# Kernel optimization log

Hardware: AMD Instinct MI355X
Metric: run time of the kernel (lower is better)

The kernel has to match this reference:

```python
import jax, jax.numpy as jnp
import numpy as np

# Sizes derived from init_kwargs via calc_mlp_features:
# total_param=2117777, router_ratio=0.002 -> router_param=4235.554, expert_param=264192
# expert_hidden = 256, router_hidden = 352
N = 131072      # number of coordinate points
CIN = 3         # expert_insize == router_insize (xyz coords)
E = 8           # num_experts
K = 2           # top_k
H = 256         # expert_hidden (also SIREN data_channel)
RH = 352        # router_hidden
NHID = 3        # expert_layers - 2 hidden SIREN layers
W0C = 30.0      # sine frequency w0


def setup_inputs() -> dict:
    key = jax.random.key(0)
    ks = jax.random.split(key, 16)
    u = lambda k, shape, a: jax.random.uniform(k, shape, jnp.float32, -a, a)
    x = jax.random.uniform(ks[0], (N, CIN), jnp.float32, -1.0, 1.0)
    context = jax.random.uniform(ks[1], (N, CIN), jnp.float32, -1.0, 1.0)
    # Router: kaiming-normal weights, torch-default uniform biases
    Wr1 = jax.random.normal(ks[2], (CIN, RH), jnp.float32) * np.float32(np.sqrt(2.0 / CIN))
    br1 = u(ks[3], (RH,), 1.0 / np.sqrt(CIN))
    Wr2 = jax.random.normal(ks[4], (RH, E), jnp.float32) * np.float32(np.sqrt(2.0 / RH))
    br2 = u(ks[5], (E,), 1.0 / np.sqrt(RH))
    # SIREN experts (stacked over E): first layer U(-1/in, 1/in), rest U(+-sqrt(6/in)/30)
    sb = np.sqrt(6.0 / H) / 30.0
    W0 = u(ks[6], (E, CIN, H), 1.0 / CIN)
    b0 = u(ks[7], (E, H), 1.0 / np.sqrt(CIN))
    Wh = u(ks[8], (E, NHID, H, H), sb)
    bh = u(ks[9], (E, NHID, H), 1.0 / np.sqrt(H))
    Wo = u(ks[10], (E, H, H), sb)
    bo = u(ks[11], (E, H), 1.0 / np.sqrt(H))
    # Decoder: Linear(H,H)+ReLU+Linear(H,1)
    Wd1 = jax.random.normal(ks[12], (H, H), jnp.float32) * np.float32(np.sqrt(2.0 / H))
    bd1 = u(ks[13], (H,), 1.0 / np.sqrt(H))
    Wd2 = jax.random.normal(ks[14], (H, 1), jnp.float32) * np.float32(np.sqrt(2.0 / H))
    bd2 = u(ks[15], (1,), 1.0 / np.sqrt(H))
    return dict(x=x, context=context, Wr1=Wr1, br1=br1, Wr2=Wr2, br2=br2,
                W0=W0, b0=b0, Wh=Wh, bh=bh, Wo=Wo, bo=bo,
                Wd1=Wd1, bd1=bd1, Wd2=Wd2, bd2=bd2)


def reference(x, context, Wr1, br1, Wr2, br2, W0, b0, Wh, bh, Wo, bo, Wd1, bd1, Wd2, bd2):
    n = x.shape[0]
    # --- NoisyTopkRouter (eval path: no noise) ---
    logits = jnp.maximum(context @ Wr1 + br1, 0.0) @ Wr2 + br2          # [N, E]
    topv, topi = jax.lax.top_k(logits, K)                                # [N, K]
    # softmax over -inf-filled sparse logits == softmax over the top-k values
    w = jax.nn.softmax(topv, axis=-1)                                    # [N, K]
    gating = jnp.zeros_like(logits).at[jnp.arange(n)[:, None], topi].set(w)  # [N, E], zero off top-k
    # --- Per-expert SIREN, weighted combine ---
    # Masked dispatch + scatter-add in the original equals dense weighted sum
    # because gating is exactly zero for non-selected experts.
    def expert_step(acc, p):
        W0e, b0e, Whe, bhe, Woe, boe, ge = p
        h = jnp.sin(W0C * (x @ W0e + b0e))                # [N, H]
        for i in range(NHID):
            h = jnp.sin(W0C * (h @ Whe[i] + bhe[i]))
        out = h @ Woe + boe                               # [N, H], no output activation
        return acc + out * ge[:, None], None
    acc0 = jnp.zeros((n, H), dtype=x.dtype)
    final, _ = jax.lax.scan(expert_step, acc0, (W0, b0, Wh, bh, Wo, bo, gating.T))
    # --- Decoder ---
    return jnp.maximum(final @ Wd1 + bd1, 0.0) @ Wd2 + bd2               # [N, 1]
```

## Files before the change

### kernel.cpp

```cpp
#include <hip/hip_runtime.h>
#include <stdint.h>

#define N_PTS 131072
#define RH    352
#define BM    256
#define BME   64
#define TPB   512
#define SREV  4.774648292756860f

typedef short  bf16x8 __attribute__((ext_vector_type(8)));
typedef float  f32x16 __attribute__((ext_vector_type(16)));

__device__ __forceinline__ unsigned short f2bf(float f) {
  uint32_t u = __builtin_bit_cast(uint32_t, f);
  u = (u + 0x7FFFu + ((u >> 16) & 1u)) >> 16;
  return (unsigned short)u;
}
__device__ __forceinline__ float bf2f(unsigned short s) {
  return __builtin_bit_cast(float, ((uint32_t)s) << 16);
}
__device__ __forceinline__ float vsin1(float x) {
  float xf = x - floorf(x);
  float r;
  asm("v_sin_f32 %0, %1" : "=v"(r) : "v"(xf));
  return r;
}
__device__ __forceinline__ void ldsload16(const void* g, void* ldsWaveBase) {
  typedef __attribute__((address_space(3))) uint8_t lds_b;
  typedef __attribute__((address_space(1))) uint8_t glob_b;
  __builtin_amdgcn_global_load_lds((const glob_b*)g, (lds_b*)ldsWaveBase, 16, 0, 0);
}
__device__ __forceinline__ f32x16 mfma_bf16(bf16x8 a, bf16x8 b, f32x16 c) {
  return __builtin_amdgcn_mfma_f32_32x32x16_bf16(a, b, c, 0, 0, 0);
}

#define AWLOAD(d0, d1, addr64) \
  asm volatile("global_load_dwordx4 %0, %2, off\n\t" \
               "global_load_dwordx4 %1, %2, off offset:1024" \
               : "=&v"(d0), "=&v"(d1) : "v"(addr64))

#define VWAIT(N, r0, r1) \
  asm volatile("s_waitcnt vmcnt(" #N ")" : "+v"(r0), "+v"(r1))

__global__ __launch_bounds__(512) void pack_kernel(
    const float* __restrict__ W0, const float* __restrict__ b0,
    const float* __restrict__ Wh, const float* __restrict__ bh,
    const float* __restrict__ Wo, const float* __restrict__ bo,
    const float* __restrict__ Wd1, const float* __restrict__ bd1,
    short* __restrict__ pW0, short* __restrict__ pWh,
    short* __restrict__ pWo, short* __restrict__ pWd1)
{
  int b = blockIdx.x, tid = threadIdx.x;
  int jb = tid >> 6, l = tid & 63;
  int j  = jb*32 + (l & 31);
  int s0 = (l >> 5) * 8;
  unsigned short o[8];
  short* dp;

  if (b < 544) {
    int m = b / 17, slice = b % 17;
    int e = m >> 2, t = m & 3;
    const float* src; const float* bias; float scale; short* dst;
    if (t < 3) { src = Wh + (size_t)(e*3+t)*65536; bias = bh + (size_t)(e*3+t)*256; scale = SREV; dst = pWh + (size_t)(e*3+t)*69632; }
    else       { src = Wo + (size_t)e*65536;       bias = bo + (size_t)e*256;       scale = 1.0f; dst = pWo + (size_t)e*69632; }
    if (slice < 16) {
      #pragma unroll
      for (int i = 0; i < 8; ++i) {
        int k = slice*16 + s0 + i;
        o[i] = f2bf(scale * src[(size_t)k*256 + j]);
      }
    } else {
      #pragma unroll
      for (int i = 0; i < 8; ++i) o[i] = 0;
      if (s0 == 0) {
        float a = scale * bias[j];
        unsigned short h = f2bf(a);
        o[0] = h; o[1] = f2bf(a - bf2f(h));
      }
    }
    dp = dst + (size_t)slice*4096 + jb*512 + l*8;
  } else if (b < 552) {
    int e = b - 544;
    const float* w0 = W0 + (size_t)e*768;
    const float* bb = b0 + (size_t)e*256;
    #pragma unroll
    for (int i = 0; i < 8; ++i) {
      int s = s0 + i;
      unsigned short v = 0;
      if (s < 3) v = f2bf(SREV * w0[(size_t)s*256 + j]);
      else if (s < 6) { float a = SREV * w0[(size_t)(s-3)*256 + j]; unsigned short h = f2bf(a); v = f2bf(a - bf2f(h)); }
      else if (s < 9) v = f2bf(SREV * w0[(size_t)(s-6)*256 + j]);
      else if (s == 9)  v = f2bf(SREV * bb[j]);
      else if (s == 10) { float a = SREV * bb[j]; unsigned short h = f2bf(a); v = f2bf(a - bf2f(h)); }
      o[i] = v;
    }
    dp = pW0 + (size_t)e*4096 + jb*512 + l*8;
  } else {
    int slice = b - 552;
    if (slice < 16) {
      #pragma unroll
      for (int i = 0; i < 8; ++i) {
        int k = slice*16 + s0 + i;
        o[i] = f2bf(Wd1[(size_t)k*256 + j]);
      }
    } else {
      #pragma unroll
      for (int i = 0; i < 8; ++i) o[i] = 0;
      if (s0 == 0) {
        float a = bd1[j];
        unsigned short h = f2bf(a);
        o[0] = h; o[1] = f2bf(a - bf2f(h));
      }
    }
    dp = pWd1 + (size_t)slice*4096 + jb*512 + l*8;
  }
  uint4 v;
  v.x = (uint32_t)o[0] | ((uint32_t)o[1] << 16);
  v.y = (uint32_t)o[2] | ((uint32_t)o[3] << 16);
  v.z = (uint32_t)o[4] | ((uint32_t)o[5] << 16);
  v.w = (uint32_t)o[6] | ((uint32_t)o[7] << 16);
  *(uint4*)dp = v;
}

__global__ __launch_bounds__(256) void router_kernel(
    const float* __restrict__ ctx, const float* __restrict__ Wr1,
    const float* __restrict__ br1, const float* __restrict__ Wr2,
    const float* __restrict__ br2, uint4* __restrict__ topk,
    uint32_t* __restrict__ counts)
{
  __shared__ double w1d[RH*4];
  __shared__ double w2d[RH*8];
  __shared__ uint32_t lcnt[8];
  int tid = threadIdx.x;
  for (int i = tid; i < RH; i += 256) {
    w1d[i*4+0] = (double)Wr1[i];
    w1d[i*4+1] = (double)Wr1[352 + i];
    w1d[i*4+2] = (double)Wr1[704 + i];
    w1d[i*4+3] = (double)br1[i];
  }
  for (int i = tid; i < RH*8; i += 256) w2d[i] = (double)Wr2[i];
  if (tid < 8) lcnt[tid] = 0;
  __syncthreads();

  int n = blockIdx.x*256 + tid;
  double c0 = (double)ctx[(size_t)n*3+0];
  double c1 = (double)ctx[(size_t)n*3+1];
  double c2 = (double)ctx[(size_t)n*3+2];
  double lg[8];
  #pragma unroll
  for (int e = 0; e < 8; ++e) lg[e] = (double)br2[e];
  for (int j = 0; j < RH; ++j) {
    const double* a = &w1d[j*4];
    double h = c0*a[0] + c1*a[1] + c2*a[2] + a[3];
    h = h > 0.0 ? h : 0.0;
    const double* bq = &w2d[j*8];
    lg[0] += h*bq[0]; lg[1] += h*bq[1]; lg[2] += h*bq[2]; lg[3] += h*bq[3];
    lg[4] += h*bq[4]; lg[5] += h*bq[5]; lg[6] += h*bq[6]; lg[7] += h*bq[7];
  }
  double v0 = -1e300, v1 = -1e300; int i0 = 0, i1 = 0;
  #pragma unroll
  for (int e = 0; e < 8; ++e) {
    double lv = lg[e];
    if (lv > v0)      { v1 = v0; i1 = i0; v0 = lv; i0 = e; }
    else if (lv > v1) { v1 = lv; i1 = e; }
  }
  float ex = __expf((float)(v1 - v0));
  float s = 1.0f / (1.0f + ex);
  uint4 t;
  t.x = (uint32_t)i0 | ((uint32_t)i1 << 8);
  t.y = __builtin_bit_cast(uint32_t, s);
  t.z = __builtin_bit_cast(uint32_t, ex * s);
  t.w = 0;
  topk[n] = t;
  atomicAdd(&lcnt[i0], 1u); atomicAdd(&lcnt[i1], 1u);
  __syncthreads();
  if (tid < 8) atomicAdd(&counts[tid], lcnt[tid]);
}

__global__ void scan_kernel(const uint32_t* __restrict__ counts,
                            uint32_t* __restrict__ offsets,
                            uint32_t* __restrict__ cursors)
{
  if (threadIdx.x == 0) {
    uint32_t o = 0;
    for (int e = 0; e < 8; ++e) { offsets[e] = o; cursors[e] = o; o += counts[e]; }
    offsets[8] = o;
  }
}

__global__ __launch_bounds__(256) void scatter_kernel(
    const uint4* __restrict__ topk, uint32_t* __restrict__ cursors,
    uint32_t* __restrict__ plist, float* __restrict__ pw)
{
  __shared__ uint32_t lc[8], lb[8];
  int tid = threadIdx.x;
  if (tid < 8) lc[tid] = 0;
  __syncthreads();
  int n = blockIdx.x*256 + tid;
  uint4 t = topk[n];
  uint32_t e0 = t.x & 255u, e1 = (t.x >> 8) & 255u;
  uint32_t p0 = atomicAdd(&lc[e0], 1u);
  uint32_t p1 = atomicAdd(&lc[e1], 1u);
  __syncthreads();
  if (tid < 8) lb[tid] = atomicAdd(&cursors[tid], lc[tid]);
  __syncthreads();
  uint32_t d0 = lb[e0] + p0, d1 = lb[e1] + p1;
  plist[d0] = ((uint32_t)n << 1);      pw[d0] = __builtin_bit_cast(float, t.y);
  plist[d1] = ((uint32_t)n << 1) | 1u; pw[d1] = __builtin_bit_cast(float, t.z);
}

__global__ __launch_bounds__(256, 3) void expert_kernel(
    const float* __restrict__ x, const uint32_t* __restrict__ counts,
    const uint32_t* __restrict__ offsets, const uint32_t* __restrict__ plist,
    const float* __restrict__ pw, const short* __restrict__ pW0,
    const short* __restrict__ pWh, const short* __restrict__ pWo,
    short* __restrict__ outbuf)
{
  __shared__ __align__(16) uint8_t smem[34816];
  uint8_t* hB = smem;
  uint8_t* xB = smem + 32768;

  int tid = threadIdx.x;
  int lane = tid & 63;
  int jq = tid >> 6;
  int aoff = jq*2048 + lane*16;

  bf16x8 bbias;
  #pragma unroll
  for (int i = 0; i < 8; ++i) bbias[i] = 0;
  if (lane < 32) { bbias[0] = (short)0x3F80; bbias[1] = (short)0x3F80; }

  bf16x8 aw[5][2];
  f32x16 acc[2][2];

  int rr = tid >> 2;
  int rq = tid & 3;

  uint32_t tt = blockIdx.x;
  int e = -1; uint32_t cnt = 0;
  #pragma unroll 1
  for (int ee = 0; ee < 8; ++ee) {
    uint32_t c = counts[ee];
    uint32_t nt = (c + (BME-1)) >> 6;
    if (tt < nt) { e = ee; cnt = c; break; }
    tt -= nt;
  }
  if (e < 0) return;
  uint32_t base = offsets[e] + (tt << 6);
  int nvalid = (int)cnt - (int)(tt << 6); if (nvalid > BME) nvalid = BME;

  uint64_t matp[4];
  matp[0] = (uint64_t)(uintptr_t)(pWh + (size_t)(e*3+0)*69632);
  matp[1] = (uint64_t)(uintptr_t)(pWh + (size_t)(e*3+1)*69632);
  matp[2] = (uint64_t)(uintptr_t)(pWh + (size_t)(e*3+2)*69632);
  matp[3] = (uint64_t)(uintptr_t)(pWo + (size_t)e*69632);

  {
    uint64_t pb = matp[0] + (uint64_t)aoff;
    AWLOAD(aw[0][0], aw[0][1], pb);
    AWLOAD(aw[1][0], aw[1][1], pb + 8192);
    AWLOAD(aw[2][0], aw[2][1], pb + 16384);
    AWLOAD(aw[3][0], aw[3][1], pb + 24576);
  }

  float wgt[2];
  #pragma unroll
  for (int c = 0; c < 2; ++c) {
    int n = c*32 + (lane & 31);
    wgt[c] = (n < nvalid) ? pw[base + n] : 0.0f;
  }
  uint32_t psv = (rr < nvalid) ? plist[base + rr] : 0u;

  if (tid < BME) {
    float x0 = 0.0f, x1 = 0.0f, x2 = 0.0f;
    if (tid < nvalid) {
      uint32_t v = plist[base + tid];
      const float* xp = x + (size_t)(v >> 1)*3;
      x0 = xp[0]; x1 = xp[1]; x2 = xp[2];
    }
    unsigned short h0 = f2bf(x0), h1 = f2bf(x1), h2 = f2bf(x2);
    unsigned short l0 = f2bf(x0 - bf2f(h0)), l1 = f2bf(x1 - bf2f(h1)), l2 = f2bf(x2 - bf2f(h2));
    uint4 r0, r1;
    r0.x = (uint32_t)h0 | ((uint32_t)h1 << 16);
    r0.y = (uint32_t)h2 | ((uint32_t)h0 << 16);
    r0.z = (uint32_t)h1 | ((uint32_t)h2 << 16);
    r0.w = (uint32_t)l0 | ((uint32_t)l1 << 16);
    r1.x = (uint32_t)l2 | (0x3F80u << 16);
    r1.y = 0x3F80u;
    r1.z = 0u; r1.w = 0u;
    uint4* dst = (uint4*)(xB + tid*32);
    dst[0] = r0; dst[1] = r1;
  }

  const uint8_t* pw0e = (const uint8_t*)(pW0 + (size_t)e*4096);
  bf16x8 a0[2];
  a0[0] = *(const bf16x8*)(pw0e + aoff);
  a0[1] = *(const bf16x8*)(pw0e + aoff + 1024);

  __syncthreads();

  #pragma unroll
  for (int a2 = 0; a2 < 2; ++a2)
    #pragma unroll
    for (int c = 0; c < 2; ++c)
      #pragma unroll
      for (int r = 0; r < 16; ++r) acc[a2][c][r] = 0.0f;

  {
    bf16x8 bv[2];
    #pragma unroll
    for (int c = 0; c < 2; ++c) {
      int n = c*32 + (lane & 31);
      bv[c] = *(const bf16x8*)(xB + n*32 + ((lane >> 5)*16));
    }
    #pragma unroll
    for (int a2 = 0; a2 < 2; ++a2)
      #pragma unroll
      for (int c = 0; c < 2; ++c)
        acc[a2][c] = mfma_bf16(a0[a2], bv[c], acc[a2][c]);
  }

  #pragma unroll
  for (int a2 = 0; a2 < 2; ++a2) {
    int jb = jq*2 + a2;
    #pragma unroll
    for (int c = 0; c < 2; ++c) {
      int n = c*32 + (lane & 31);
      uint32_t rowb = (uint32_t)n * 512u;
      uint32_t sw = (uint32_t)((n & 7) << 4);
      #pragma unroll
      for (int g = 0; g < 4; ++g) {
        float s0f = vsin1(acc[a2][c][g*4+0]);
        float s1f = vsin1(acc[a2][c][g*4+1]);
        float s2f = vsin1(acc[a2][c][g*4+2]);
        float s3f = vsin1(acc[a2][c][g*4+3]);
        uint2 pv;
        pv.x = (uint32_t)f2bf(s0f) | ((uint32_t)f2bf(s1f) << 16);
        pv.y = (uint32_t)f2bf(s2f) | ((uint32_t)f2bf(s3f) << 16);
        int j0 = jb*32 + g*8 + ((lane >> 5) << 2);
        uint32_t off = (rowb + (uint32_t)(j0*2)) ^ sw;
        *(uint2*)(hB + off) = pv;
      }
    }
  }
  __syncthreads();

#define STEP(L, kb) { \
    enum { u_ = (L)*17 + (kb), ps_ = u_ + 4, us_ = u_ % 5, pss_ = ps_ % 5 }; \
    if (ps_ <= 67) { \
      uint64_t pa_ = matp[ps_/17] + (uint64_t)((ps_%17)*8192) + (uint64_t)aoff; \
      AWLOAD(aw[pss_][0], aw[pss_][1], pa_); \
    } \
    if (u_ <= 63)      { VWAIT(8, aw[us_][0], aw[us_][1]); } \
    else if (u_ == 64) { VWAIT(6, aw[us_][0], aw[us_][1]); } \
    else if (u_ == 65) { VWAIT(4, aw[us_][0], aw[us_][1]); } \
    else if (u_ == 66) { VWAIT(2, aw[us_][0], aw[us_][1]); } \
    else               { VWAIT(0, aw[us_][0], aw[us_][1]); } \
    bf16x8 bv0_, bv1_; \
    if ((kb) < 16) { \
      { int n_ = (lane & 31); \
        uint32_t off_ = ((uint32_t)n_*512u + (uint32_t)((kb)*32) + (uint32_t)((lane >> 5)*16)) \
                        ^ (uint32_t)((n_ & 7) << 4); \
        bv0_ = *(const bf16x8*)(hB + off_); } \
      { int n_ = 32 + (lane & 31); \
        uint32_t off_ = ((uint32_t)n_*512u + (uint32_t)((kb)*32) + (uint32_t)((lane >> 5)*16)) \
                        ^ (uint32_t)((n_ & 7) << 4); \
        bv1_ = *(const bf16x8*)(hB + off_); } \
    } else { bv0_ = bbias; bv1_ = bbias; } \
    acc[0][0] = mfma_bf16(aw[us_][0], bv0_, acc[0][0]); \
    acc[1][0] = mfma_bf16(aw[us_][1], bv0_, acc[1][0]); \
    acc[0][1] = mfma_bf16(aw[us_][0], bv1_, acc[0][1]); \
    acc[1][1] = mfma_bf16(aw[us_][1], bv1_, acc[1][1]); \
}
#define LAYER17(L) STEP(L,0) STEP(L,1) STEP(L,2) STEP(L,3) STEP(L,4) STEP(L,5) \
    STEP(L,6) STEP(L,7) STEP(L,8) STEP(L,9) STEP(L,10) STEP(L,11) STEP(L,12) \
    STEP(L,13) STEP(L,14) STEP(L,15) STEP(L,16)

#define ZACC() { _Pragma("unroll") for (int a2 = 0; a2 < 2; ++a2) \
    _Pragma("unroll") for (int c = 0; c < 2; ++c) \
    _Pragma("unroll") for (int r = 0; r < 16; ++r) acc[a2][c][r] = 0.0f; }

#define WRITE_SIN() { _Pragma("unroll") \
    for (int a2 = 0; a2 < 2; ++a2) { \
      int jb = jq*2 + a2; \
      _Pragma("unroll") \
      for (int c = 0; c < 2; ++c) { \
        int n = c*32 + (lane & 31); \
        uint32_t rowb = (uint32_t)n * 512u; \
        uint32_t sw = (uint32_t)((n & 7) << 4); \
        _Pragma("unroll") \
        for (int g = 0; g < 4; ++g) { \
          float s0f = vsin1(acc[a2][c][g*4+0]); \
          float s1f = vsin1(acc[a2][c][g*4+1]); \
          float s2f = vsin1(acc[a2][c][g*4+2]); \
          float s3f = vsin1(acc[a2][c][g*4+3]); \
          uint2 pv; \
          pv.x = (uint32_t)f2bf(s0f) | ((uint32_t)f2bf(s1f) << 16); \
          pv.y = (uint32_t)f2bf(s2f) | ((uint32_t)f2bf(s3f) << 16); \
          int j0 = jb*32 + g*8 + ((lane >> 5) << 2); \
          uint32_t off = (rowb + (uint32_t)(j0*2)) ^ sw; \
          *(uint2*)(hB + off) = pv; \
        } \
      } \
    } }

  ZACC(); LAYER17(0)
  __syncthreads(); WRITE_SIN(); __syncthreads();
  ZACC(); LAYER17(1)
  __syncthreads(); WRITE_SIN(); __syncthreads();
  ZACC(); LAYER17(2)
  __syncthreads(); WRITE_SIN(); __syncthreads();
  ZACC(); LAYER17(3)
  __syncthreads();
  #pragma unroll
  for (int a2 = 0; a2 < 2; ++a2) {
    int jb = jq*2 + a2;
    #pragma unroll
    for (int c = 0; c < 2; ++c) {
      int n = c*32 + (lane & 31);
      float w = wgt[c];
      uint32_t rowb = (uint32_t)n * 512u;
      uint32_t sw = (uint32_t)((n & 7) << 4);
      #pragma unroll
      for (int g = 0; g < 4; ++g) {
        float s0f = acc[a2][c][g*4+0] * w;
        float s1f = acc[a2][c][g*4+1] * w;
        float s2f = acc[a2][c][g*4+2] * w;
        float s3f = acc[a2][c][g*4+3] * w;
        uint2 pv;
        pv.x = (uint32_t)f2bf(s0f) | ((uint32_t)f2bf(s1f) << 16);
        pv.y = (uint32_t)f2bf(s2f) | ((uint32_t)f2bf(s3f) << 16);
        int j0 = jb*32 + g*8 + ((lane >> 5) << 2);
        uint32_t off = (rowb + (uint32_t)(j0*2)) ^ sw;
        *(uint2*)(hB + off) = pv;
      }
    }
  }
  __syncthreads();
  if (rr < nvalid) {
    uint4* dst = (uint4*)(outbuf + ((size_t)(psv & 1)*N_PTS + (size_t)(psv >> 1))*256);
    uint32_t rowb = (uint32_t)rr*512u;
    uint32_t sw = (uint32_t)((rr & 7) << 4);
    #pragma unroll
    for (int c = 0; c < 8; ++c) {
      int ch = c*4 + rq;
      dst[ch] = *(const uint4*)(hB + ((rowb + (uint32_t)(ch*16)) ^ sw));
    }
  }
}

#define LDS_DEC 150528

__global__ __launch_bounds__(TPB, 2) void decoder_kernel(
    const short* __restrict__ outbuf, const short* __restrict__ pWd1,
    const float* __restrict__ Wd2v, const float* __restrict__ bd2,
    float* __restrict__ outp)
{
  extern __shared__ __align__(16) uint8_t smem[];
  uint8_t* hB = smem;
  uint8_t* wB = smem + 131072;
  float* wd2 = (float*)(smem + 147456);
  float* part = (float*)(smem + 148480);

  int tid = threadIdx.x;
  int lane = tid & 63;
  int wv = tid >> 6;
  int nw = wv & 3;
  int jw = wv >> 2;
  int tbase = blockIdx.x * BM;

  ldsload16((const uint8_t*)pWd1 + (size_t)tid*16, wB + (tid >> 6)*1024);
  if (tid < 256) wd2[tid] = Wd2v[tid];

  const short* o0 = outbuf + (size_t)tbase*256;
  const short* o1 = outbuf + ((size_t)N_PTS + tbase)*256;
  #pragma unroll 1
  for (int it = 0; it < 16; ++it) {
    int c = it*512 + tid;
    uint4 a  = *(const uint4*)(o0 + (size_t)c*8);
    uint4 bq = *(const uint4*)(o1 + (size_t)c*8);
    uint4 ov;
    uint32_t* ap = (uint32_t*)&a;
    uint32_t* bp = (uint32_t*)&bq;
    uint32_t* op = (uint32_t*)&ov;
    #pragma unroll
    for (int w = 0; w < 4; ++w) {
      uint32_t ua = ap[w], ub = bp[w];
      float f0 = bf2f((unsigned short)(ua & 0xFFFFu)) + bf2f((unsigned short)(ub & 0xFFFFu));
      float f1 = bf2f((unsigned short)(ua >> 16))     + bf2f((unsigned short)(ub >> 16));
      op[w] = (uint32_t)f2bf(f0) | ((uint32_t)f2bf(f1) << 16);
    }
    int n = c >> 5;
    uint32_t off = ((uint32_t)n*512u + (uint32_t)(c & 31)*16u) ^ (uint32_t)((n & 7) << 4);
    *(uint4*)(hB + off) = ov;
  }
  __syncthreads();

  f32x16 acc[4][2];
  #pragma unroll
  for (int a2 = 0; a2 < 4; ++a2)
    #pragma unroll
    for (int c = 0; c < 2; ++c)
      #pragma unroll
      for (int r = 0; r < 16; ++r) acc[a2][c][r] = 0.0f;
  bf16x8 bbias;
  #pragma unroll
  for (int i = 0; i < 8; ++i) bbias[i] = 0;
  if (lane < 32) { bbias[0] = (short)0x3F80; bbias[1] = (short)0x3F80; }

  #pragma unroll 1
  for (int kb = 0; kb < 17; ++kb) {
    if (kb < 16)
      ldsload16((const uint8_t*)(pWd1 + (size_t)(kb+1)*4096) + (size_t)tid*16,
                wB + ((kb+1) & 1)*8192 + (tid >> 6)*1024);
    const uint8_t* wcur = wB + (kb & 1)*8192;
    bf16x8 av[4];
    #pragma unroll
    for (int a2 = 0; a2 < 4; ++a2)
      av[a2] = *(const bf16x8*)(wcur + (jw*4 + a2)*1024 + lane*16);
    bf16x8 bv[2];
    if (kb < 16) {
      #pragma unroll
      for (int c = 0; c < 2; ++c) {
        int n = (nw*2 + c)*32 + (lane & 31);
        uint32_t off = ((uint32_t)n*512u + (uint32_t)kb*32u + (uint32_t)((lane >> 5)*16))
                       ^ (uint32_t)((n & 7) << 4);
        bv[c] = *(const bf16x8*)(hB + off);
      }
    } else {
      bv[0] = bbias; bv[1] = bbias;
    }
    #pragma unroll
    for (int a2 = 0; a2 < 4; ++a2)
      #pragma unroll
      for (int c = 0; c < 2; ++c)
        acc[a2][c] = mfma_bf16(av[a2], bv[c], acc[a2][c]);
    __syncthreads();
  }

  float p0 = 0.0f, p1 = 0.0f;
  #pragma unroll
  for (int a2 = 0; a2 < 4; ++a2) {
    int jb = jw*4 + a2;
    #pragma unroll
    for (int c = 0; c < 2; ++c) {
      #pragma unroll
      for (int r = 0; r < 16; ++r) {
        int j = jb*32 + (r & 3) + ((r >> 2) << 3) + ((lane >> 5) << 2);
        float v = acc[a2][c][r];
        v = v > 0.0f ? v : 0.0f;
        float t = v * wd2[j];
        if (c == 0) p0 += t; else p1 += t;
      }
    }
  }
  p0 += __shfl_xor(p0, 32);
  p1 += __shfl_xor(p1, 32);
  if (lane < 32) {
    part[jw*256 + (nw*2+0)*32 + lane] = p0;
    part[jw*256 + (nw*2+1)*32 + lane] = p1;
  }
  __syncthreads();
  if (tid < 256)
    outp[tbase + tid] = part[tid] + part[256 + tid] + bd2[0];
}

extern "C" void kernel_launch(void* const* d_in, const int* in_sizes, int n_in,
                              void* d_out, int out_size, void* d_ws, size_t ws_size,
                              hipStream_t stream) {
  const float* x   = (const float*)d_in[0];
  const float* ctx = (const float*)d_in[1];
  const float* Wr1 = (const float*)d_in[2];
  const float* br1 = (const float*)d_in[3];
  const float* Wr2 = (const float*)d_in[4];
  const float* br2 = (const float*)d_in[5];
  const float* W0  = (const float*)d_in[6];
  const float* b0  = (const float*)d_in[7];
  const float* Wh  = (const float*)d_in[8];
  const float* bh  = (const float*)d_in[9];
  const float* Wo  = (const float*)d_in[10];
  const float* bo  = (const float*)d_in[11];
  const float* Wd1 = (const float*)d_in[12];
  const float* bd1 = (const float*)d_in[13];
  const float* Wd2 = (const float*)d_in[14];
  const float* bd2 = (const float*)d_in[15];
  float* out = (float*)d_out;

  const size_t WS_COUNTS  = 0;
  const size_t WS_CURSORS = 256;
  const size_t WS_OFFSETS = 512;
  const size_t WS_TOPK    = 1024;
  const size_t WS_PLIST   = WS_TOPK  + (size_t)N_PTS*16;
  const size_t WS_PW      = WS_PLIST + (size_t)N_PTS*8;
  const size_t WS_PW0     = WS_PW    + (size_t)N_PTS*8;
  const size_t WS_PWH     = WS_PW0   + (size_t)8*8192;
  const size_t WS_PWO     = WS_PWH   + (size_t)24*139264;
  const size_t WS_PWD1    = WS_PWO   + (size_t)8*139264;
  const size_t WS_OUT     = WS_PWD1  + (size_t)139264;
  const size_t WS_END     = WS_OUT   + (size_t)2*N_PTS*256*2;

  if (ws_size < WS_END) {
    hipMemsetAsync(d_out, 0xFF, (size_t)out_size*4, stream);
    return;
  }

  uint8_t* ws = (uint8_t*)d_ws;
  uint32_t* counts  = (uint32_t*)(ws + WS_COUNTS);
  uint32_t* cursors = (uint32_t*)(ws + WS_CURSORS);
  uint32_t* offsets = (uint32_t*)(ws + WS_OFFSETS);
  uint4*    topk    = (uint4*)   (ws + WS_TOPK);
  uint32_t* plist   = (uint32_t*)(ws + WS_PLIST);
  float*    pw      = (float*)   (ws + WS_PW);
  short*    pW0     = (short*)   (ws + WS_PW0);
  short*    pWh     = (short*)   (ws + WS_PWH);
  short*    pWo     = (short*)   (ws + WS_PWO);
  short*    pWd1    = (short*)   (ws + WS_PWD1);
  short*    outbuf  = (short*)   (ws + WS_OUT);

  hipMemsetAsync(counts, 0, 32, stream);
  hipFuncSetAttribute((const void*)decoder_kernel,
                      hipFuncAttributeMaxDynamicSharedMemorySize, LDS_DEC);

  pack_kernel   <<<569,  512, 0, stream>>>(W0, b0, Wh, bh, Wo, bo, Wd1, bd1,
                                           pW0, pWh, pWo, pWd1);
  router_kernel <<<512,  256, 0, stream>>>(ctx, Wr1, br1, Wr2, br2, topk, counts);
  scan_kernel   <<<1,     64, 0, stream>>>(counts, offsets, cursors);
  scatter_kernel<<<512,  256, 0, stream>>>(topk, cursors, plist, pw);
  expert_kernel <<<4104, 256, 0, stream>>>(x, counts, offsets, plist, pw,
                                           pW0, pWh, pWo, outbuf);
  decoder_kernel<<<512,  TPB, LDS_DEC, stream>>>(outbuf, pWd1, Wd2, bd2, out);
}
```

Before: 275.4 us.

## Merge pack and router kernels, drop scan kernel, restructure decoder with register-streamed weights

The weight-packing and router kernels become a single launch, and the scan kernel is removed: scatter and expert kernels now compute per-expert offsets from counts directly, and cursors start at zero via a widened memset. The decoder is rewritten to use 64-row blocks with 256 threads and static LDS. It streams Wd1 slices into registers through a 4-deep global-load pipeline instead of double-buffered LDS. This cuts launch count and inter-kernel gaps and raises decoder occupancy, at the cost of each block reloading all of Wd1 from global memory or cache.

```diff
diff --git a/kernel.cpp b/kernel.cpp
--- a/kernel.cpp
+++ b/kernel.cpp
@@ -3,9 +3,6 @@
 
 #define N_PTS 131072
 #define RH    352
-#define BM    256
-#define BME   64
-#define TPB   512
 #define SREV  4.774648292756860f
 
 typedef short  bf16x8 __attribute__((ext_vector_type(8)));
@@ -25,11 +22,6 @@
   asm("v_sin_f32 %0, %1" : "=v"(r) : "v"(xf));
   return r;
 }
-__device__ __forceinline__ void ldsload16(const void* g, void* ldsWaveBase) {
-  typedef __attribute__((address_space(3))) uint8_t lds_b;
-  typedef __attribute__((address_space(1))) uint8_t glob_b;
-  __builtin_amdgcn_global_load_lds((const glob_b*)g, (lds_b*)ldsWaveBase, 16, 0, 0);
-}
 __device__ __forceinline__ f32x16 mfma_bf16(bf16x8 a, bf16x8 b, f32x16 c) {
   return __builtin_amdgcn_mfma_f32_32x32x16_bf16(a, b, c, 0, 0, 0);
 }
@@ -42,87 +34,13 @@
 #define VWAIT(N, r0, r1) \
   asm volatile("s_waitcnt vmcnt(" #N ")" : "+v"(r0), "+v"(r1))
 
-__global__ __launch_bounds__(512) void pack_kernel(
+__global__ __launch_bounds__(512) void setup_kernel(
     const float* __restrict__ W0, const float* __restrict__ b0,
     const float* __restrict__ Wh, const float* __restrict__ bh,
     const float* __restrict__ Wo, const float* __restrict__ bo,
     const float* __restrict__ Wd1, const float* __restrict__ bd1,
     short* __restrict__ pW0, short* __restrict__ pWh,
-    short* __restrict__ pWo, short* __restrict__ pWd1)
-{
-  int b = blockIdx.x, tid = threadIdx.x;
-  int jb = tid >> 6, l = tid & 63;
-  int j  = jb*32 + (l & 31);
-  int s0 = (l >> 5) * 8;
-  unsigned short o[8];
-  short* dp;
-
-  if (b < 544) {
-    int m = b / 17, slice = b % 17;
-    int e = m >> 2, t = m & 3;
-    const float* src; const float* bias; float scale; short* dst;
-    if (t < 3) { src = Wh + (size_t)(e*3+t)*65536; bias = bh + (size_t)(e*3+t)*256; scale = SREV; dst = pWh + (size_t)(e*3+t)*69632; }
-    else       { src = Wo + (size_t)e*65536;       bias = bo + (size_t)e*256;       scale = 1.0f; dst = pWo + (size_t)e*69632; }
-    if (slice < 16) {
-      #pragma unroll
-      for (int i = 0; i < 8; ++i) {
-        int k = slice*16 + s0 + i;
-        o[i] = f2bf(scale * src[(size_t)k*256 + j]);
-      }
-    } else {
-      #pragma unroll
-      for (int i = 0; i < 8; ++i) o[i] = 0;
-      if (s0 == 0) {
-        float a = scale * bias[j];
-        unsigned short h = f2bf(a);
-        o[0] = h; o[1] = f2bf(a - bf2f(h));
-      }
-    }
-    dp = dst + (size_t)slice*4096 + jb*512 + l*8;
-  } else if (b < 552) {
-    int e = b - 544;
-    const float* w0 = W0 + (size_t)e*768;
-    const float* bb = b0 + (size_t)e*256;
-    #pragma unroll
-    for (int i = 0; i < 8; ++i) {
-      int s = s0 + i;
-      unsigned short v = 0;
-      if (s < 3) v = f2bf(SREV * w0[(size_t)s*256 + j]);
-      else if (s < 6) { float a = SREV * w0[(size_t)(s-3)*256 + j]; unsigned short h = f2bf(a); v = f2bf(a - bf2f(h)); }
-      else if (s < 9) v = f2bf(SREV * w0[(size_t)(s-6)*256 + j]);
-      else if (s == 9)  v = f2bf(SREV * bb[j]);
-      else if (s == 10) { float a = SREV * bb[j]; unsigned short h = f2bf(a); v = f2bf(a - bf2f(h)); }
-      o[i] = v;
-    }
-    dp = pW0 + (size_t)e*4096 + jb*512 + l*8;
-  } else {
-    int slice = b - 552;
-    if (slice < 16) {
-      #pragma unroll
-      for (int i = 0; i < 8; ++i) {
-        int k = slice*16 + s0 + i;
-        o[i] = f2bf(Wd1[(size_t)k*256 + j]);
-      }
-    } else {
-      #pragma unroll
-      for (int i = 0; i < 8; ++i) o[i] = 0;
-      if (s0 == 0) {
-        float a = bd1[j];
-        unsigned short h = f2bf(a);
-        o[0] = h; o[1] = f2bf(a - bf2f(h));
-      }
-    }
-    dp = pWd1 + (size_t)slice*4096 + jb*512 + l*8;
-  }
-  uint4 v;
-  v.x = (uint32_t)o[0] | ((uint32_t)o[1] << 16);
-  v.y = (uint32_t)o[2] | ((uint32_t)o[3] << 16);
-  v.z = (uint32_t)o[4] | ((uint32_t)o[5] << 16);
-  v.w = (uint32_t)o[6] | ((uint32_t)o[7] << 16);
-  *(uint4*)dp = v;
-}
-
-__global__ __launch_bounds__(256) void router_kernel(
+    short* __restrict__ pWo, short* __restrict__ pWd1,
     const float* __restrict__ ctx, const float* __restrict__ Wr1,
     const float* __restrict__ br1, const float* __restrict__ Wr2,
     const float* __restrict__ br2, uint4* __restrict__ topk,
@@ -131,18 +49,92 @@
   __shared__ double w1d[RH*4];
   __shared__ double w2d[RH*8];
   __shared__ uint32_t lcnt[8];
-  int tid = threadIdx.x;
-  for (int i = tid; i < RH; i += 256) {
+  int b = blockIdx.x, tid = threadIdx.x;
+
+  if (b < 569) {
+    int jb = tid >> 6, l = tid & 63;
+    int j  = jb*32 + (l & 31);
+    int s0 = (l >> 5) * 8;
+    unsigned short o[8];
+    short* dp;
+    if (b < 544) {
+      int m = b / 17, slice = b % 17;
+      int e = m >> 2, t = m & 3;
+      const float* src; const float* bias; float scale; short* dst;
+      if (t < 3) { src = Wh + (size_t)(e*3+t)*65536; bias = bh + (size_t)(e*3+t)*256; scale = SREV; dst = pWh + (size_t)(e*3+t)*69632; }
+      else       { src = Wo + (size_t)e*65536;       bias = bo + (size_t)e*256;       scale = 1.0f; dst = pWo + (size_t)e*69632; }
+      if (slice < 16) {
+        #pragma unroll
+        for (int i = 0; i < 8; ++i) {
+          int k = slice*16 + s0 + i;
+          o[i] = f2bf(scale * src[(size_t)k*256 + j]);
+        }
+      } else {
+        #pragma unroll
+        for (int i = 0; i < 8; ++i) o[i] = 0;
+        if (s0 == 0) {
+          float a = scale * bias[j];
+          unsigned short h = f2bf(a);
+          o[0] = h; o[1] = f2bf(a - bf2f(h));
+        }
+      }
+      dp = dst + (size_t)slice*4096 + jb*512 + l*8;
+    } else if (b < 552) {
+      int e = b - 544;
+      const float* w0 = W0 + (size_t)e*768;
+      const float* bb = b0 + (size_t)e*256;
+      #pragma unroll
+      for (int i = 0; i < 8; ++i) {
+        int s = s0 + i;
+        unsigned short v = 0;
+        if (s < 3) v = f2bf(SREV * w0[(size_t)s*256 + j]);
+        else if (s < 6) { float a = SREV * w0[(size_t)(s-3)*256 + j]; unsigned short h = f2bf(a); v = f2bf(a - bf2f(h)); }
+        else if (s < 9) v = f2bf(SREV * w0[(size_t)(s-6)*256 + j]);
+        else if (s == 9)  v = f2bf(SREV * bb[j]);
+        else if (s == 10) { float a = SREV * bb[j]; unsigned short h = f2bf(a); v = f2bf(a - bf2f(h)); }
+        o[i] = v;
+      }
+      dp = pW0 + (size_t)e*4096 + jb*512 + l*8;
+    } else {
+      int slice = b - 552;
+      if (slice < 16) {
+        #pragma unroll
+        for (int i = 0; i < 8; ++i) {
+          int k = slice*16 + s0 + i;
+          o[i] = f2bf(Wd1[(size_t)k*256 + j]);
+        }
+      } else {
+        #pragma unroll
+        for (int i = 0; i < 8; ++i) o[i] = 0;
+        if (s0 == 0) {
+          float a = bd1[j];
+          unsigned short h = f2bf(a);
+          o[0] = h; o[1] = f2bf(a - bf2f(h));
+        }
+      }
+      dp = pWd1 + (size_t)slice*4096 + jb*512 + l*8;
+    }
+    uint4 v;
+    v.x = (uint32_t)o[0] | ((uint32_t)o[1] << 16);
+    v.y = (uint32_t)o[2] | ((uint32_t)o[3] << 16);
+    v.z = (uint32_t)o[4] | ((uint32_t)o[5] << 16);
+    v.w = (uint32_t)o[6] | ((uint32_t)o[7] << 16);
+    *(uint4*)dp = v;
+    return;
+  }
+
+  int rb = b - 569;
+  for (int i = tid; i < RH; i += 512) {
     w1d[i*4+0] = (double)Wr1[i];
     w1d[i*4+1] = (double)Wr1[352 + i];
     w1d[i*4+2] = (double)Wr1[704 + i];
     w1d[i*4+3] = (double)br1[i];
   }
-  for (int i = tid; i < RH*8; i += 256) w2d[i] = (double)Wr2[i];
+  for (int i = tid; i < RH*8; i += 512) w2d[i] = (double)Wr2[i];
   if (tid < 8) lcnt[tid] = 0;
   __syncthreads();
 
-  int n = blockIdx.x*256 + tid;
+  int n = rb*512 + tid;
   double c0 = (double)ctx[(size_t)n*3+0];
   double c1 = (double)ctx[(size_t)n*3+1];
   double c2 = (double)ctx[(size_t)n*3+2];
@@ -177,24 +169,19 @@
   if (tid < 8) atomicAdd(&counts[tid], lcnt[tid]);
 }
 
-__global__ void scan_kernel(const uint32_t* __restrict__ counts,
-                            uint32_t* __restrict__ offsets,
-                            uint32_t* __restrict__ cursors)
+__global__ __launch_bounds__(256) void scatter_kernel(
+    const uint4* __restrict__ topk, const uint32_t* __restrict__ counts,
+    uint32_t* __restrict__ cursors, uint32_t* __restrict__ plist,
+    float* __restrict__ pw)
 {
-  if (threadIdx.x == 0) {
+  __shared__ uint32_t lc[8], lb[8], offs[8];
+  int tid = threadIdx.x;
+  if (tid < 8) {
+    lc[tid] = 0;
     uint32_t o = 0;
-    for (int e = 0; e < 8; ++e) { offsets[e] = o; cursors[e] = o; o += counts[e]; }
-    offsets[8] = o;
-  }
-}
-
-__global__ __launch_bounds__(256) void scatter_kernel(
-    const uint4* __restrict__ topk, uint32_t* __restrict__ cursors,
-    uint32_t* __restrict__ plist, float* __restrict__ pw)
-{
-  __shared__ uint32_t lc[8], lb[8];
-  int tid = threadIdx.x;
-  if (tid < 8) lc[tid] = 0;
+    for (int k = 0; k < tid; ++k) o += counts[k];
+    offs[tid] = o;
+  }
   __syncthreads();
   int n = blockIdx.x*256 + tid;
   uint4 t = topk[n];
@@ -202,7 +189,7 @@
   uint32_t p0 = atomicAdd(&lc[e0], 1u);
   uint32_t p1 = atomicAdd(&lc[e1], 1u);
   __syncthreads();
-  if (tid < 8) lb[tid] = atomicAdd(&cursors[tid], lc[tid]);
+  if (tid < 8) lb[tid] = offs[tid] + atomicAdd(&cursors[tid], lc[tid]);
   __syncthreads();
   uint32_t d0 = lb[e0] + p0, d1 = lb[e1] + p1;
   plist[d0] = ((uint32_t)n << 1);      pw[d0] = __builtin_bit_cast(float, t.y);
@@ -211,10 +198,9 @@
 
 __global__ __launch_bounds__(256, 3) void expert_kernel(
     const float* __restrict__ x, const uint32_t* __restrict__ counts,
-    const uint32_t* __restrict__ offsets, const uint32_t* __restrict__ plist,
-    const float* __restrict__ pw, const short* __restrict__ pW0,
-    const short* __restrict__ pWh, const short* __restrict__ pWo,
-    short* __restrict__ outbuf)
+    const uint32_t* __restrict__ plist, const float* __restrict__ pw,
+    const short* __restrict__ pW0, const short* __restrict__ pWh,
+    const short* __restrict__ pWo, short* __restrict__ outbuf)
 {
   __shared__ __align__(16) uint8_t smem[34816];
   uint8_t* hB = smem;
@@ -237,17 +223,17 @@
   int rq = tid & 3;
 
   uint32_t tt = blockIdx.x;
-  int e = -1; uint32_t cnt = 0;
+  int e = -1; uint32_t cnt = 0, off = 0;
   #pragma unroll 1
   for (int ee = 0; ee < 8; ++ee) {
     uint32_t c = counts[ee];
-    uint32_t nt = (c + (BME-1)) >> 6;
+    uint32_t nt = (c + 63u) >> 6;
     if (tt < nt) { e = ee; cnt = c; break; }
-    tt -= nt;
+    tt -= nt; off += c;
   }
   if (e < 0) return;
-  uint32_t base = offsets[e] + (tt << 6);
-  int nvalid = (int)cnt - (int)(tt << 6); if (nvalid > BME) nvalid = BME;
+  uint32_t base = off + (tt << 6);
+  int nvalid = (int)cnt - (int)(tt << 6); if (nvalid > 64) nvalid = 64;
 
   uint64_t matp[4];
   matp[0] = (uint64_t)(uintptr_t)(pWh + (size_t)(e*3+0)*69632);
@@ -271,7 +257,7 @@
   }
   uint32_t psv = (rr < nvalid) ? plist[base + rr] : 0u;
 
-  if (tid < BME) {
+  if (tid < 64) {
     float x0 = 0.0f, x1 = 0.0f, x2 = 0.0f;
     if (tid < nvalid) {
       uint32_t v = plist[base + tid];
@@ -320,29 +306,31 @@
         acc[a2][c] = mfma_bf16(a0[a2], bv[c], acc[a2][c]);
   }
 
-  #pragma unroll
-  for (int a2 = 0; a2 < 2; ++a2) {
-    int jb = jq*2 + a2;
-    #pragma unroll
-    for (int c = 0; c < 2; ++c) {
-      int n = c*32 + (lane & 31);
-      uint32_t rowb = (uint32_t)n * 512u;
-      uint32_t sw = (uint32_t)((n & 7) << 4);
-      #pragma unroll
-      for (int g = 0; g < 4; ++g) {
-        float s0f = vsin1(acc[a2][c][g*4+0]);
-        float s1f = vsin1(acc[a2][c][g*4+1]);
-        float s2f = vsin1(acc[a2][c][g*4+2]);
-        float s3f = vsin1(acc[a2][c][g*4+3]);
-        uint2 pv;
-        pv.x = (uint32_t)f2bf(s0f) | ((uint32_t)f2bf(s1f) << 16);
-        pv.y = (uint32_t)f2bf(s2f) | ((uint32_t)f2bf(s3f) << 16);
-        int j0 = jb*32 + g*8 + ((lane >> 5) << 2);
-        uint32_t off = (rowb + (uint32_t)(j0*2)) ^ sw;
-        *(uint2*)(hB + off) = pv;
-      }
-    }
-  }
+#define WRITE_SIN() { _Pragma("unroll") \
+    for (int a2 = 0; a2 < 2; ++a2) { \
+      int jb = jq*2 + a2; \
+      _Pragma("unroll") \
+      for (int c = 0; c < 2; ++c) { \
+        int n = c*32 + (lane & 31); \
+        uint32_t rowb = (uint32_t)n * 512u; \
+        uint32_t sw = (uint32_t)((n & 7) << 4); \
+        _Pragma("unroll") \
+        for (int g = 0; g < 4; ++g) { \
+          float s0f = vsin1(acc[a2][c][g*4+0]); \
+          float s1f = vsin1(acc[a2][c][g*4+1]); \
+          float s2f = vsin1(acc[a2][c][g*4+2]); \
+          float s3f = vsin1(acc[a2][c][g*4+3]); \
+          uint2 pv; \
+          pv.x = (uint32_t)f2bf(s0f) | ((uint32_t)f2bf(s1f) << 16); \
+          pv.y = (uint32_t)f2bf(s2f) | ((uint32_t)f2bf(s3f) << 16); \
+          int j0 = jb*32 + g*8 + ((lane >> 5) << 2); \
+          uint32_t off2 = (rowb + (uint32_t)(j0*2)) ^ sw; \
+          *(uint2*)(hB + off2) = pv; \
+        } \
+      } \
+    } }
+
+  WRITE_SIN();
   __syncthreads();
 
 #define STEP(L, kb) { \
@@ -380,30 +368,6 @@
     _Pragma("unroll") for (int c = 0; c < 2; ++c) \
     _Pragma("unroll") for (int r = 0; r < 16; ++r) acc[a2][c][r] = 0.0f; }
 
-#define WRITE_SIN() { _Pragma("unroll") \
-    for (int a2 = 0; a2 < 2; ++a2) { \
-      int jb = jq*2 + a2; \
-      _Pragma("unroll") \
-      for (int c = 0; c < 2; ++c) { \
-        int n = c*32 + (lane & 31); \
-        uint32_t rowb = (uint32_t)n * 512u; \
-        uint32_t sw = (uint32_t)((n & 7) << 4); \
-        _Pragma("unroll") \
-        for (int g = 0; g < 4; ++g) { \
-          float s0f = vsin1(acc[a2][c][g*4+0]); \
-          float s1f = vsin1(acc[a2][c][g*4+1]); \
-          float s2f = vsin1(acc[a2][c][g*4+2]); \
-          float s3f = vsin1(acc[a2][c][g*4+3]); \
-          uint2 pv; \
-          pv.x = (uint32_t)f2bf(s0f) | ((uint32_t)f2bf(s1f) << 16); \
-          pv.y = (uint32_t)f2bf(s2f) | ((uint32_t)f2bf(s3f) << 16); \
-          int j0 = jb*32 + g*8 + ((lane >> 5) << 2); \
-          uint32_t off = (rowb + (uint32_t)(j0*2)) ^ sw; \
-          *(uint2*)(hB + off) = pv; \
-        } \
-      } \
-    } }
-
   ZACC(); LAYER17(0)
   __syncthreads(); WRITE_SIN(); __syncthreads();
   ZACC(); LAYER17(1)
@@ -431,117 +395,127 @@
         pv.x = (uint32_t)f2bf(s0f) | ((uint32_t)f2bf(s1f) << 16);
         pv.y = (uint32_t)f2bf(s2f) | ((uint32_t)f2bf(s3f) << 16);
         int j0 = jb*32 + g*8 + ((lane >> 5) << 2);
-        uint32_t off = (rowb + (uint32_t)(j0*2)) ^ sw;
-        *(uint2*)(hB + off) = pv;
+        uint32_t off2 = (rowb + (uint32_t)(j0*2)) ^ sw;
+        *(uint2*)(hB + off2) = pv;
       }
     }
   }
   __syncthreads();
   if (rr < nvalid) {
-    uint4* dst = (uint4*)(outbuf + ((size_t)(psv & 1)*N_PTS + (size_t)(psv >> 1))*256);
-    uint32_t rowb = (uint32_t)rr*512u;
+    uint4* dst = (uint4*)(outbuf + ((size_t)(psv & 1)*N_PTS + (size_t)(psv >> 1))*256
+                          + rq*64);
+    uint32_t rowb = (uint32_t)rr*512u + (uint32_t)rq*128u;
     uint32_t sw = (uint32_t)((rr & 7) << 4);
     #pragma unroll
-    for (int c = 0; c < 8; ++c) {
-      int ch = c*4 + rq;
-      dst[ch] = *(const uint4*)(hB + ((rowb + (uint32_t)(ch*16)) ^ sw));
-    }
-  }
-}
-
-#define LDS_DEC 150528
-
-__global__ __launch_bounds__(TPB, 2) void decoder_kernel(
+    for (int c = 0; c < 8; ++c)
+      dst[c] = *(const uint4*)(hB + ((rowb + (uint32_t)(c*16)) ^ sw));
+  }
+}
+
+__global__ __launch_bounds__(256, 3) void decoder_kernel(
     const short* __restrict__ outbuf, const short* __restrict__ pWd1,
     const float* __restrict__ Wd2v, const float* __restrict__ bd2,
     float* __restrict__ outp)
 {
-  extern __shared__ __align__(16) uint8_t smem[];
+  __shared__ __align__(16) uint8_t smem[34816];
   uint8_t* hB = smem;
-  uint8_t* wB = smem + 131072;
-  float* wd2 = (float*)(smem + 147456);
-  float* part = (float*)(smem + 148480);
+  float* wd2  = (float*)(smem + 32768);
+  float* part = (float*)(smem + 33792);
 
   int tid = threadIdx.x;
   int lane = tid & 63;
-  int wv = tid >> 6;
-  int nw = wv & 3;
-  int jw = wv >> 2;
-  int tbase = blockIdx.x * BM;
-
-  ldsload16((const uint8_t*)pWd1 + (size_t)tid*16, wB + (tid >> 6)*1024);
-  if (tid < 256) wd2[tid] = Wd2v[tid];
-
-  const short* o0 = outbuf + (size_t)tbase*256;
-  const short* o1 = outbuf + ((size_t)N_PTS + tbase)*256;
-  #pragma unroll 1
-  for (int it = 0; it < 16; ++it) {
-    int c = it*512 + tid;
-    uint4 a  = *(const uint4*)(o0 + (size_t)c*8);
-    uint4 bq = *(const uint4*)(o1 + (size_t)c*8);
-    uint4 ov;
-    uint32_t* ap = (uint32_t*)&a;
-    uint32_t* bp = (uint32_t*)&bq;
-    uint32_t* op = (uint32_t*)&ov;
-    #pragma unroll
-    for (int w = 0; w < 4; ++w) {
-      uint32_t ua = ap[w], ub = bp[w];
-      float f0 = bf2f((unsigned short)(ua & 0xFFFFu)) + bf2f((unsigned short)(ub & 0xFFFFu));
-      float f1 = bf2f((unsigned short)(ua >> 16))     + bf2f((unsigned short)(ub >> 16));
-      op[w] = (uint32_t)f2bf(f0) | ((uint32_t)f2bf(f1) << 16);
+  int jq = tid >> 6;
+  int aoff = jq*2048 + lane*16;
+  int tbase = blockIdx.x * 64;
+  int rr = tid >> 2;
+  int rq = tid & 3;
+
+  bf16x8 bbias;
+  #pragma unroll
+  for (int i = 0; i < 8; ++i) bbias[i] = 0;
+  if (lane < 32) { bbias[0] = (short)0x3F80; bbias[1] = (short)0x3F80; }
+
+  bf16x8 aw[5][2];
+  f32x16 acc[2][2];
+
+  uint64_t wp = (uint64_t)(uintptr_t)pWd1;
+  {
+    uint64_t pb = wp + (uint64_t)aoff;
+    AWLOAD(aw[0][0], aw[0][1], pb);
+    AWLOAD(aw[1][0], aw[1][1], pb + 8192);
+    AWLOAD(aw[2][0], aw[2][1], pb + 16384);
+    AWLOAD(aw[3][0], aw[3][1], pb + 24576);
+  }
+
+  wd2[tid] = Wd2v[tid];
+
+  {
+    const short* o0 = outbuf + (size_t)(tbase + rr)*256 + rq*64;
+    const short* o1 = o0 + (size_t)N_PTS*256;
+    uint32_t rowb = (uint32_t)rr*512u + (uint32_t)rq*128u;
+    uint32_t sw = (uint32_t)((rr & 7) << 4);
+    #pragma unroll
+    for (int c = 0; c < 8; ++c) {
+      uint4 a  = *(const uint4*)(o0 + c*8);
+      uint4 bq = *(const uint4*)(o1 + c*8);
+      uint4 ov;
+      uint32_t* ap = (uint32_t*)&a;
+      uint32_t* bp = (uint32_t*)&bq;
+      uint32_t* op = (uint32_t*)&ov;
+      #pragma unroll
+      for (int w = 0; w < 4; ++w) {
+        uint32_t ua = ap[w], ub = bp[w];
+        float f0 = bf2f((unsigned short)(ua & 0xFFFFu)) + bf2f((unsigned short)(ub & 0xFFFFu));
+        float f1 = bf2f((unsigned short)(ua >> 16))     + bf2f((unsigned short)(ub >> 16));
+        op[w] = (uint32_t)f2bf(f0) | ((uint32_t)f2bf(f1) << 16);
+      }
+      *(uint4*)(hB + ((rowb + (uint32_t)(c*16)) ^ sw)) = ov;
     }
-    int n = c >> 5;
-    uint32_t off = ((uint32_t)n*512u + (uint32_t)(c & 31)*16u) ^ (uint32_t)((n & 7) << 4);
-    *(uint4*)(hB + off) = ov;
-  }
-  __syncthreads();
-
-  f32x16 acc[4][2];
-  #pragma unroll
-  for (int a2 = 0; a2 < 4; ++a2)
+  }
+  __syncthreads();
+
+  #pragma unroll
+  for (int a2 = 0; a2 < 2; ++a2)
     #pragma unroll
     for (int c = 0; c < 2; ++c)
       #pragma unroll
       for (int r = 0; r < 16; ++r) acc[a2][c][r] = 0.0f;
-  bf16x8 bbias;
-  #pragma unroll
-  for (int i = 0; i < 8; ++i) bbias[i] = 0;
-  if (lane < 32) { bbias[0] = (short)0x3F80; bbias[1] = (short)0x3F80; }
-
-  #pragma unroll 1
-  for (int kb = 0; kb < 17; ++kb) {
-    if (kb < 16)
-      ldsload16((const uint8_t*)(pWd1 + (size_t)(kb+1)*4096) + (size_t)tid*16,
-                wB + ((kb+1) & 1)*8192 + (tid >> 6)*1024);
-    const uint8_t* wcur = wB + (kb & 1)*8192;
-    bf16x8 av[4];
-    #pragma unroll
-    for (int a2 = 0; a2 < 4; ++a2)
-      av[a2] = *(const bf16x8*)(wcur + (jw*4 + a2)*1024 + lane*16);
-    bf16x8 bv[2];
-    if (kb < 16) {
-      #pragma unroll
-      for (int c = 0; c < 2; ++c) {
-        int n = (nw*2 + c)*32 + (lane & 31);
-        uint32_t off = ((uint32_t)n*512u + (uint32_t)kb*32u + (uint32_t)((lane >> 5)*16))
-                       ^ (uint32_t)((n & 7) << 4);
-        bv[c] = *(const bf16x8*)(hB + off);
-      }
-    } else {
-      bv[0] = bbias; bv[1] = bbias;
-    }
-    #pragma unroll
-    for (int a2 = 0; a2 < 4; ++a2)
-      #pragma unroll
-      for (int c = 0; c < 2; ++c)
-        acc[a2][c] = mfma_bf16(av[a2], bv[c], acc[a2][c]);
-    __syncthreads();
-  }
+
+#define DSTEP(kb) { \
+    enum { ps_ = (kb) + 4, us_ = (kb) % 5, pss_ = ps_ % 5 }; \
+    if (ps_ <= 16) { \
+      uint64_t pa_ = wp + (uint64_t)(ps_*8192) + (uint64_t)aoff; \
+      AWLOAD(aw[pss_][0], aw[pss_][1], pa_); \
+    } \
+    if ((kb) <= 12)      { VWAIT(8, aw[us_][0], aw[us_][1]); } \
+    else if ((kb) == 13) { VWAIT(6, aw[us_][0], aw[us_][1]); } \
+    else if ((kb) == 14) { VWAIT(4, aw[us_][0], aw[us_][1]); } \
+    else if ((kb) == 15) { VWAIT(2, aw[us_][0], aw[us_][1]); } \
+    else                 { VWAIT(0, aw[us_][0], aw[us_][1]); } \
+    bf16x8 bv0_, bv1_; \
+    if ((kb) < 16) { \
+      { int n_ = (lane & 31); \
+        uint32_t off_ = ((uint32_t)n_*512u + (uint32_t)((kb)*32) + (uint32_t)((lane >> 5)*16)) \
+                        ^ (uint32_t)((n_ & 7) << 4); \
+        bv0_ = *(const bf16x8*)(hB + off_); } \
+      { int n_ = 32 + (lane & 31); \
+        uint32_t off_ = ((uint32_t)n_*512u + (uint32_t)((kb)*32) + (uint32_t)((lane >> 5)*16)) \
+                        ^ (uint32_t)((n_ & 7) << 4); \
+        bv1_ = *(const bf16x8*)(hB + off_); } \
+    } else { bv0_ = bbias; bv1_ = bbias; } \
+    acc[0][0] = mfma_bf16(aw[us_][0], bv0_, acc[0][0]); \
+    acc[1][0] = mfma_bf16(aw[us_][1], bv0_, acc[1][0]); \
+    acc[0][1] = mfma_bf16(aw[us_][0], bv1_, acc[0][1]); \
+    acc[1][1] = mfma_bf16(aw[us_][1], bv1_, acc[1][1]); \
+}
+  DSTEP(0)  DSTEP(1)  DSTEP(2)  DSTEP(3)  DSTEP(4)  DSTEP(5)
+  DSTEP(6)  DSTEP(7)  DSTEP(8)  DSTEP(9)  DSTEP(10) DSTEP(11)
+  DSTEP(12) DSTEP(13) DSTEP(14) DSTEP(15) DSTEP(16)
 
   float p0 = 0.0f, p1 = 0.0f;
   #pragma unroll
-  for (int a2 = 0; a2 < 4; ++a2) {
-    int jb = jw*4 + a2;
+  for (int a2 = 0; a2 < 2; ++a2) {
+    int jb = jq*2 + a2;
     #pragma unroll
     for (int c = 0; c < 2; ++c) {
       #pragma unroll
@@ -557,12 +531,13 @@
   p0 += __shfl_xor(p0, 32);
   p1 += __shfl_xor(p1, 32);
   if (lane < 32) {
-    part[jw*256 + (nw*2+0)*32 + lane] = p0;
-    part[jw*256 + (nw*2+1)*32 + lane] = p1;
-  }
-  __syncthreads();
-  if (tid < 256)
-    outp[tbase + tid] = part[tid] + part[256 + tid] + bd2[0];
+    part[jq*64 + lane] = p0;
+    part[jq*64 + 32 + lane] = p1;
+  }
+  __syncthreads();
+  if (tid < 64)
+    outp[tbase + tid] = part[tid] + part[64 + tid] + part[128 + tid]
+                      + part[192 + tid] + bd2[0];
 }
 
 extern "C" void kernel_launch(void* const* d_in, const int* in_sizes, int n_in,
@@ -587,8 +562,7 @@
   float* out = (float*)d_out;
 
   const size_t WS_COUNTS  = 0;
-  const size_t WS_CURSORS = 256;
-  const size_t WS_OFFSETS = 512;
+  const size_t WS_CURSORS = 32;
   const size_t WS_TOPK    = 1024;
   const size_t WS_PLIST   = WS_TOPK  + (size_t)N_PTS*16;
   const size_t WS_PW      = WS_PLIST + (size_t)N_PTS*8;
@@ -607,7 +581,6 @@
   uint8_t* ws = (uint8_t*)d_ws;
   uint32_t* counts  = (uint32_t*)(ws + WS_COUNTS);
   uint32_t* cursors = (uint32_t*)(ws + WS_CURSORS);
-  uint32_t* offsets = (uint32_t*)(ws + WS_OFFSETS);
   uint4*    topk    = (uint4*)   (ws + WS_TOPK);
   uint32_t* plist   = (uint32_t*)(ws + WS_PLIST);
   float*    pw      = (float*)   (ws + WS_PW);
@@ -617,16 +590,13 @@
   short*    pWd1    = (short*)   (ws + WS_PWD1);
   short*    outbuf  = (short*)   (ws + WS_OUT);
 
-  hipMemsetAsync(counts, 0, 32, stream);
-  hipFuncSetAttribute((const void*)decoder_kernel,
-                      hipFuncAttributeMaxDynamicSharedMemorySize, LDS_DEC);
-
-  pack_kernel   <<<569,  512, 0, stream>>>(W0, b0, Wh, bh, Wo, bo, Wd1, bd1,
-                                           pW0, pWh, pWo, pWd1);
-  router_kernel <<<512,  256, 0, stream>>>(ctx, Wr1, br1, Wr2, br2, topk, counts);
-  scan_kernel   <<<1,     64, 0, stream>>>(counts, offsets, cursors);
-  scatter_kernel<<<512,  256, 0, stream>>>(topk, cursors, plist, pw);
-  expert_kernel <<<4104, 256, 0, stream>>>(x, counts, offsets, plist, pw,
+  hipMemsetAsync(counts, 0, 64, stream);
+
+  setup_kernel  <<<825,  512, 0, stream>>>(W0, b0, Wh, bh, Wo, bo, Wd1, bd1,
+                                           pW0, pWh, pWo, pWd1,
+                                           ctx, Wr1, br1, Wr2, br2, topk, counts);
+  scatter_kernel<<<512,  256, 0, stream>>>(topk, counts, cursors, plist, pw);
+  expert_kernel <<<4104, 256, 0, stream>>>(x, counts, plist, pw,
                                            pW0, pWh, pWo, outbuf);
-  decoder_kernel<<<512,  TPB, LDS_DEC, stream>>>(outbuf, pWd1, Wd2, bd2, out);
-}
+  decoder_kernel<<<2048, 256, 0, stream>>>(outbuf, pWd1, Wd2, bd2, out);
+}
```

Result: no change. 279.1 us (+1.3%).
